# Performance work log

Hardware: AMD Instinct MI355X
Metric: run time of the kernel (lower is better)

## Reference

```python
import jax, jax.numpy as jnp
import numpy as np

N_NODES = 100000
N_EDGES = 1600000
D = 128
NUM_LAYERS = 3
BN_EPS = 1e-5


def setup_inputs() -> dict:
    key = jax.random.key(0)
    k1, k2, k3 = jax.random.split(key, 3)
    x = jax.random.normal(k1, (N_NODES, D), dtype=jnp.float32)
    edge_index = jax.random.randint(k2, (2, N_EDGES), 0, N_NODES, dtype=jnp.int32)
    # xavier-uniform-ish scale for relu gain
    scale = jnp.sqrt(2.0) * jnp.sqrt(6.0 / (D + D))
    Ws = jax.random.uniform(k3, (NUM_LAYERS, D, D), dtype=jnp.float32, minval=-1.0, maxval=1.0) * scale
    gammas = jnp.ones((NUM_LAYERS - 1, D), dtype=jnp.float32)
    betas = jnp.zeros((NUM_LAYERS - 1, D), dtype=jnp.float32)
    return {"x": x, "edge_index": edge_index, "Ws": Ws, "gammas": gammas, "betas": betas}


def gcn_conv(x, W, src, dst, num_nodes):
    # GCNConv(normalize=False, bias=False): linear then scatter-add aggregation
    h = x @ W                               # [N, D]
    msgs = h[src]                           # [E, D] irregular gather
    return jax.ops.segment_sum(msgs, dst, num_segments=num_nodes)  # [N, D] scatter-add


def batch_norm(x, gamma, beta):
    # training-mode BN over node dim, biased variance (torch semantics), deterministic
    mu = jnp.mean(x, axis=0)
    var = jnp.var(x, axis=0)
    return (x - mu) * jax.lax.rsqrt(var + BN_EPS) * gamma + beta


def reference(x, edge_index, Ws, gammas, betas):
    src, dst = edge_index[0], edge_index[1]
    n = x.shape[0]
    for i in range(NUM_LAYERS):
        x = gcn_conv(x, Ws[i], src, dst, n)
        if i != NUM_LAYERS - 1:
            x = batch_norm(x, gammas[i], betas[i])
            x = jax.nn.relu(x)
            # dropout omitted for a deterministic reference (eval-equivalent)
    return jax.nn.log_softmax(x, axis=-1)
```

## Files before the change

### kernel.cpp

```cpp
#include <hip/hip_runtime.h>

#define BN_EPS 1e-5f

typedef __attribute__((ext_vector_type(8))) short bf16x8;
typedef __attribute__((ext_vector_type(4))) float f32x4;

union VU {
    uint4 u;
    bf16x8 b;
};


__global__ __launch_bounds__(256) void hist_k(const int* __restrict__ dst, int E,
                                              int* __restrict__ ghist, int NB) {
    __shared__ int lh[128];
    if (threadIdx.x < 128) lh[threadIdx.x] = 0;
    __syncthreads();
    for (int i = blockIdx.x * 256 + threadIdx.x; i < E; i += gridDim.x * 256)
        atomicAdd(&lh[dst[i] >> 10], 1);
    __syncthreads();
    if (threadIdx.x < NB && lh[threadIdx.x]) atomicAdd(&ghist[threadIdx.x * 16], lh[threadIdx.x]);
}

__global__ __launch_bounds__(128) void pscan_k(const int* __restrict__ ghist, int NB,
                                               int* __restrict__ sbase, int* __restrict__ csrB,
                                               int* __restrict__ rowptr, int n, int E) {
    __shared__ int pa[128], pc[128];
    int t = threadIdx.x;
    int v = (t < NB) ? ghist[t * 16] : 0;
    int vp = (v + 15) & ~15;
    pa[t] = vp;
    pc[t] = v;
    __syncthreads();
    for (int s = 1; s < 128; s <<= 1) {
        int ta = (t >= s) ? pa[t - s] : 0;
        int tc = (t >= s) ? pc[t - s] : 0;
        __syncthreads();
        pa[t] += ta;
        pc[t] += tc;
        __syncthreads();
    }
    if (t < NB) {
        sbase[t] = pa[t] - vp;
        csrB[t] = pc[t] - v;
        if (t == NB - 1) {
            csrB[NB] = pc[t];
            rowptr[n] = E;
        }
    }
}

#define CHUNK 2048
__global__ __launch_bounds__(256) void bin_k(const int* __restrict__ src, const int* __restrict__ dst, int E,
                                             const int* __restrict__ sbase, int* __restrict__ snext,
                                             int* __restrict__ staged, int NB) {
    __shared__ int hist[128];
    __shared__ int base[128];
    int t = threadIdx.x;
    int c0 = blockIdx.x * CHUNK;
    if (c0 >= E) return;
    if (t < 128) hist[t] = 0;
    __syncthreads();
    int bk[8], pk[8], rk[8];
#pragma unroll
    for (int k = 0; k < 8; ++k) {
        int i = c0 + k * 256 + t;
        bk[k] = -1;
        if (i < E) {
            int d = dst[i];
            int b = d >> 10;
            bk[k] = b;
            pk[k] = src[i] | ((d & 1023) << 17);
            rk[k] = atomicAdd(&hist[b], 1);
        }
    }
    __syncthreads();
    if (t < NB) base[t] = sbase[t] + atomicAdd(&snext[t * 16], hist[t]);
    __syncthreads();
#pragma unroll
    for (int k = 0; k < 8; ++k)
        if (bk[k] >= 0) staged[base[bk[k]] + rk[k]] = pk[k];
}

__global__ __launch_bounds__(1024) void csr_k(const int* __restrict__ staged, const int* __restrict__ ghist,
                                              const int* __restrict__ sbase, const int* __restrict__ csrB,
                                              int* __restrict__ rowptr, int* __restrict__ ssrc, int n) {
    __shared__ int hist[1024], cur[1024];
    int b = blockIdx.x, t = threadIdx.x;
    int nodeBase = b << 10;
    hist[t] = 0;
    __syncthreads();
    int s0 = sbase[b], c = ghist[b * 16];
    for (int j = t; j < c; j += 1024) atomicAdd(&hist[staged[s0 + j] >> 17], 1);
    __syncthreads();
    int v = hist[t];
    for (int s = 1; s < 1024; s <<= 1) {
        int tv = (t >= s) ? hist[t - s] : 0;
        __syncthreads();
        hist[t] += tv;
        __syncthreads();
    }
    int ex = hist[t] - v;
    int cb = csrB[b];
    if (nodeBase + t < n) rowptr[nodeBase + t] = cb + ex;
    cur[t] = ex;
    __syncthreads();
    for (int j = t; j < c; j += 1024) {
        int e = staged[s0 + j];
        int p = atomicAdd(&cur[e >> 17], 1);
        ssrc[cb + p] = e & 131071;
    }
}


static __device__ __forceinline__ unsigned short f2bf(float f) {
    unsigned u = __float_as_uint(f);
    unsigned r = (u + 0x7FFFu + ((u >> 16) & 1u)) >> 16;
    return (unsigned short)r;
}
static __device__ __forceinline__ float bf_lo(unsigned u) { return __uint_as_float(u << 16); }
static __device__ __forceinline__ float bf_hi(unsigned u) { return __uint_as_float(u & 0xFFFF0000u); }


__global__ __launch_bounds__(256) void prepw_k(const float* __restrict__ Ws, uint4* __restrict__ Wp) {
    int id = blockIdx.x * 256 + threadIdx.x;
    if (id >= 3 * 4 * 8 * 64) return;
    int lane = id & 63;
    int nt = (id >> 6) & 7;
    int kt = (id >> 9) & 3;
    int L = id >> 11;
    int quad = lane >> 4, l16 = lane & 15;
    const float* wsrc = Ws + L * 16384 + (kt * 32 + quad * 8) * 128 + nt * 16 + l16;
    unsigned short s[8];
#pragma unroll
    for (int j = 0; j < 8; ++j) s[j] = f2bf(wsrc[j * 128]);
    uint4 pk;
    pk.x = (unsigned)s[0] | ((unsigned)s[1] << 16);
    pk.y = (unsigned)s[2] | ((unsigned)s[3] << 16);
    pk.z = (unsigned)s[4] | ((unsigned)s[5] << 16);
    pk.w = (unsigned)s[6] | ((unsigned)s[7] << 16);
    Wp[id] = pk;
}


template <int MODE>
__global__ __launch_bounds__(256) void mgemm_k(const float* __restrict__ Xf, const unsigned short* __restrict__ Xb,
                                               const uint4* __restrict__ Wp, unsigned short* __restrict__ H,
                                               const float* __restrict__ ss, int n) {
    int lane = threadIdx.x & 63;
    int quad = lane >> 4, l16 = lane & 15;
    int wid = (blockIdx.x * 256 + threadIdx.x) >> 6;
    int nw = (gridDim.x * 256) >> 6;
    int ntiles = (n + 15) >> 4;

    VU b[4][8];
#pragma unroll
    for (int kt = 0; kt < 4; ++kt)
#pragma unroll
        for (int nt = 0; nt < 8; ++nt) b[kt][nt].u = Wp[(kt * 8 + nt) * 64 + lane];

    auto loadA = [&](int tile, VU* a) {
        int row = tile * 16 + l16;
#pragma unroll
        for (int kt = 0; kt < 4; ++kt) {
            float f[8];
            if (MODE == 0) {
                const float* xr = Xf + (size_t)row * 128 + kt * 32 + quad * 8;
                float4 u0 = *(const float4*)(xr);
                float4 u1 = *(const float4*)(xr + 4);
                f[0] = u0.x; f[1] = u0.y; f[2] = u0.z; f[3] = u0.w;
                f[4] = u1.x; f[5] = u1.y; f[6] = u1.z; f[7] = u1.w;
            } else {
                int sl = kt * 2 + (quad >> 1);
                uint4 u = *(const uint4*)(Xb + ((size_t)sl * n + row) * 16 + (quad & 1) * 8);
                f[0] = bf_lo(u.x); f[1] = bf_hi(u.x); f[2] = bf_lo(u.y); f[3] = bf_hi(u.y);
                f[4] = bf_lo(u.z); f[5] = bf_hi(u.z); f[6] = bf_lo(u.w); f[7] = bf_hi(u.w);
                const float4* scp = (const float4*)(ss + kt * 32 + quad * 8);
                const float4* shp = (const float4*)(ss + 128 + kt * 32 + quad * 8);
                float4 c0 = scp[0], c1 = scp[1], d0 = shp[0], d1 = shp[1];
                f[0] = fmaxf(fmaf(f[0], c0.x, d0.x), 0.f);
                f[1] = fmaxf(fmaf(f[1], c0.y, d0.y), 0.f);
                f[2] = fmaxf(fmaf(f[2], c0.z, d0.z), 0.f);
                f[3] = fmaxf(fmaf(f[3], c0.w, d0.w), 0.f);
                f[4] = fmaxf(fmaf(f[4], c1.x, d1.x), 0.f);
                f[5] = fmaxf(fmaf(f[5], c1.y, d1.y), 0.f);
                f[6] = fmaxf(fmaf(f[6], c1.z, d1.z), 0.f);
                f[7] = fmaxf(fmaf(f[7], c1.w, d1.w), 0.f);
            }
            uint4 pk;
            pk.x = (unsigned)f2bf(f[0]) | ((unsigned)f2bf(f[1]) << 16);
            pk.y = (unsigned)f2bf(f[2]) | ((unsigned)f2bf(f[3]) << 16);
            pk.z = (unsigned)f2bf(f[4]) | ((unsigned)f2bf(f[5]) << 16);
            pk.w = (unsigned)f2bf(f[6]) | ((unsigned)f2bf(f[7]) << 16);
            a[kt].u = pk;
        }
    };

    int t = wid;
    VU a[4];
    if (t < ntiles) loadA(t, a);

    while (t < ntiles) {
        int tn = t + nw;
        VU an[4];
        if (tn < ntiles) loadA(tn, an);

        f32x4 acc[8];
#pragma unroll
        for (int nt = 0; nt < 8; ++nt) acc[nt] = (f32x4){0.f, 0.f, 0.f, 0.f};
#pragma unroll
        for (int kt = 0; kt < 4; ++kt)
#pragma unroll
            for (int nt = 0; nt < 8; ++nt)
                acc[nt] = __builtin_amdgcn_mfma_f32_16x16x32_bf16(b[kt][nt].b, a[kt].b, acc[nt], 0, 0, 0);

        int row = t * 16 + l16;
#pragma unroll
        for (int nt = 0; nt < 8; ++nt) {
            uint2 pk;
            pk.x = (unsigned)f2bf(acc[nt][0]) | ((unsigned)f2bf(acc[nt][1]) << 16);
            pk.y = (unsigned)f2bf(acc[nt][2]) | ((unsigned)f2bf(acc[nt][3]) << 16);
            *(uint2*)(H + ((size_t)nt * n + row) * 16 + quad * 4) = pk;
        }

#pragma unroll
        for (int kt = 0; kt < 4; ++kt) a[kt] = an[kt];
        t = tn;
    }
}


template <int MODE>
__global__ __launch_bounds__(256) void aggs_k(const unsigned short* __restrict__ H, const int* __restrict__ rowptr,
                                              const int* __restrict__ ssrc, unsigned* __restrict__ outb,
                                              float* __restrict__ outf, float* __restrict__ stats, int n) {
    __shared__ float sred[4][4][8];
    int slice = blockIdx.x & 7;
    int bg = blockIdx.x >> 3;
    int lane = threadIdx.x & 63;
    int wv = threadIdx.x >> 6;
    int g = lane >> 3;
    int f = lane & 7;
    int wid = bg * 4 + wv;
    int nwave = (gridDim.x >> 3) * 4;
    const unsigned short* hs = H + (size_t)slice * n * 16 + f * 2;
    float s0 = 0, s1 = 0, q0 = 0, q1 = 0;

    for (int base = wid * 8; base < n; base += nwave * 8) {
        int node = base + g;
        bool valid = node < n;
        int cn = valid ? node : (n - 1);
        int beg = rowptr[cn];
        int end = valid ? rowptr[cn + 1] : beg;
        float ax = 0.f, ay = 0.f;

        for (int s = 0;; s += 8) {
            if (__ballot((beg + s) < end) == 0) break;
            int idx[8];
            float sc[8];
#pragma unroll
            for (int k = 0; k < 8; ++k) {
                int j = beg + s + k;
                int cj = j < end ? j : end - 1;
                cj = cj < 0 ? 0 : cj;
                idx[k] = ssrc[cj];
                sc[k] = (j < end) ? 1.f : 0.f;
            }
            unsigned v[8];
#pragma unroll
            for (int k = 0; k < 8; ++k) v[k] = *(const unsigned*)(hs + (size_t)idx[k] * 16);
#pragma unroll
            for (int k = 0; k < 8; ++k) {
                ax = fmaf(sc[k], bf_lo(v[k]), ax);
                ay = fmaf(sc[k], bf_hi(v[k]), ay);
            }
        }

        if (MODE == 0) {
            if (valid) outb[((size_t)slice * n + node) * 8 + f] = (unsigned)f2bf(ax) | ((unsigned)f2bf(ay) << 16);
            s0 += ax; q0 += ax * ax;
            s1 += ay; q1 += ay * ay;
        } else {
            if (valid) *(float2*)(outf + (size_t)node * 128 + slice * 16 + f * 2) = make_float2(ax, ay);
        }
    }

    if (MODE == 0) {
        s0 += __shfl_xor(s0, 8); s0 += __shfl_xor(s0, 16); s0 += __shfl_xor(s0, 32);
        s1 += __shfl_xor(s1, 8); s1 += __shfl_xor(s1, 16); s1 += __shfl_xor(s1, 32);
        q0 += __shfl_xor(q0, 8); q0 += __shfl_xor(q0, 16); q0 += __shfl_xor(q0, 32);
        q1 += __shfl_xor(q1, 8); q1 += __shfl_xor(q1, 16); q1 += __shfl_xor(q1, 32);
        if (g == 0) {
            sred[wv][0][f] = s0;
            sred[wv][1][f] = s1;
            sred[wv][2][f] = q0;
            sred[wv][3][f] = q1;
        }
        __syncthreads();
        if (wv == 0 && g == 0) {
            float t0 = (sred[0][0][f] + sred[1][0][f]) + (sred[2][0][f] + sred[3][0][f]);
            float t1 = (sred[0][1][f] + sred[1][1][f]) + (sred[2][1][f] + sred[3][1][f]);
            float t2 = (sred[0][2][f] + sred[1][2][f]) + (sred[2][2][f] + sred[3][2][f]);
            float t3 = (sred[0][3][f] + sred[1][3][f]) + (sred[2][3][f] + sred[3][3][f]);
            atomicAdd(&stats[slice * 16 + 2 * f], t0);
            atomicAdd(&stats[slice * 16 + 2 * f + 1], t1);
            atomicAdd(&stats[128 + slice * 16 + 2 * f], t2);
            atomicAdd(&stats[128 + slice * 16 + 2 * f + 1], t3);
        }
    }
}


__global__ __launch_bounds__(256) void lsm_k(float* __restrict__ out, int n) {
    int lane = threadIdx.x & 63;
    int wid = (blockIdx.x * 256 + threadIdx.x) >> 6;
    int nw = (gridDim.x * 256) >> 6;
    for (int node = wid; node < n; node += nw) {
        float2 v = *(float2*)(out + (size_t)node * 128 + 2 * lane);
        float m = fmaxf(v.x, v.y);
#pragma unroll
        for (int off = 32; off > 0; off >>= 1) m = fmaxf(m, __shfl_xor(m, off));
        float ex = expf(v.x - m) + expf(v.y - m);
#pragma unroll
        for (int off = 32; off > 0; off >>= 1) ex += __shfl_xor(ex, off);
        float lse = m + logf(ex);
        *(float2*)(out + (size_t)node * 128 + 2 * lane) = make_float2(v.x - lse, v.y - lse);
    }
}


__global__ void bnfin_k(const float* __restrict__ stats, const float* __restrict__ gamma,
                        const float* __restrict__ beta, float* __restrict__ ss, int n) {
    int f = threadIdx.x;
    if (f < 128) {
        float mu = stats[f] / n;
        float var = stats[128 + f] / n - mu * mu;
        float rs = rsqrtf(fmaxf(var, 0.f) + BN_EPS);
        float sc = gamma[f] * rs;
        ss[f] = sc;
        ss[128 + f] = beta[f] - mu * sc;
    }
}


extern "C" void kernel_launch(void* const* d_in, const int* in_sizes, int n_in,
                              void* d_out, int out_size, void* d_ws, size_t ws_size,
                              hipStream_t stream) {
    const float* x = (const float*)d_in[0];
    const int* ei = (const int*)d_in[1];
    const float* Ws = (const float*)d_in[2];
    const float* gammas = (const float*)d_in[3];
    const float* betas = (const float*)d_in[4];
    int N = in_sizes[0] / 128;
    int E = in_sizes[1] / 2;
    const int* src = ei;
    const int* dst = ei + E;
    float* out = (float*)d_out;

    char* w = (char*)d_ws;
    size_t o = 0;
    auto alloc = [&](size_t bytes) { char* p = w + o; o += (bytes + 511) & ~511ull; return p; };
    unsigned short* h = (unsigned short*)alloc((size_t)N * 128 * 2);
    unsigned short* h2 = (unsigned short*)alloc((size_t)N * 128 * 2);
    int* rowptr = (int*)alloc(((size_t)N + 1) * 4);
    int* ssrc = (int*)alloc((size_t)E * 4);
    uint4* Wp = (uint4*)alloc(3 * 2048 * 16);
    float* stats = (float*)alloc(512 * 4);
    float* ss = (float*)alloc(512 * 4);

    int NB = (N + 1023) >> 10;
    int* ghist = (int*)alloc((size_t)NB * 16 * 4);
    int* snext = (int*)alloc((size_t)NB * 16 * 4);
    int* sbase = (int*)alloc((size_t)NB * 4);
    int* csrB = (int*)alloc(((size_t)NB + 1) * 4);
    int* staged = (int*)h2;

    hipMemsetAsync(ghist, 0, (size_t)NB * 16 * 4, stream);
    hipMemsetAsync(snext, 0, (size_t)NB * 16 * 4, stream);
    hipMemsetAsync(stats, 0, 512 * 4, stream);

    prepw_k<<<24, 256, 0, stream>>>(Ws, Wp);
    hist_k<<<256, 256, 0, stream>>>(dst, E, ghist, NB);
    pscan_k<<<1, 128, 0, stream>>>(ghist, NB, sbase, csrB, rowptr, N, E);
    bin_k<<<(E + CHUNK - 1) / CHUNK, 256, 0, stream>>>(src, dst, E, sbase, snext, staged, NB);
    csr_k<<<NB, 1024, 0, stream>>>(staged, ghist, sbase, csrB, rowptr, ssrc, N);

    const int AGG_BLOCKS = 2048;
    const int GEMM_BLOCKS = 512;

    mgemm_k<0><<<GEMM_BLOCKS, 256, 0, stream>>>(x, nullptr, Wp, h, nullptr, N);
    aggs_k<0><<<AGG_BLOCKS, 256, 0, stream>>>(h, rowptr, ssrc, (unsigned*)h2, nullptr, stats, N);
    bnfin_k<<<1, 128, 0, stream>>>(stats, gammas, betas, ss, N);
    mgemm_k<1><<<GEMM_BLOCKS, 256, 0, stream>>>(nullptr, h2, Wp + 2048, h, ss, N);
    aggs_k<0><<<AGG_BLOCKS, 256, 0, stream>>>(h, rowptr, ssrc, (unsigned*)h2, nullptr, stats + 256, N);
    bnfin_k<<<1, 128, 0, stream>>>(stats + 256, gammas + 128, betas + 128, ss + 256, N);
    mgemm_k<1><<<GEMM_BLOCKS, 256, 0, stream>>>(nullptr, h2, Wp + 4096, h, ss + 256, N);
    aggs_k<1><<<AGG_BLOCKS, 256, 0, stream>>>(h, rowptr, ssrc, nullptr, out, nullptr, N);
    lsm_k<<<1024, 256, 0, stream>>>(out, N);
}
```

Measured before the change: 513.3 us.

## Widen aggregation gathers to 8 bytes and cooperatively load indices via shuffles

The aggregation kernel now assigns 4 lanes per node, each gathering 4 bf16 features (8 bytes) instead of 8 lanes with 4-byte loads, so each wave handles 16 nodes at once. Neighbor indices are loaded cooperatively (one per lane), broadcast with shuffles, and prefetched one iteration ahead. The ssrc buffer gains a zero-filled pad so the over-reads stay in bounds. Together these aim to cut redundant index loads and the number of memory transactions in the gather-bound phase, at the cost of extra shuffles and possibly lower memory-level parallelism per node.

Result: slower. 564.2 us (+9.9%).

```diff
diff --git a/kernel.cpp b/kernel.cpp
--- a/kernel.cpp
+++ b/kernel.cpp
@@ -239,73 +239,88 @@
     int bg = blockIdx.x >> 3;
     int lane = threadIdx.x & 63;
     int wv = threadIdx.x >> 6;
-    int g = lane >> 3;
-    int f = lane & 7;
+    int g = lane >> 2;
+    int f4 = lane & 3;
     int wid = bg * 4 + wv;
     int nwave = (gridDim.x >> 3) * 4;
-    const unsigned short* hs = H + (size_t)slice * n * 16 + f * 2;
-    float s0 = 0, s1 = 0, q0 = 0, q1 = 0;
-
-    for (int base = wid * 8; base < n; base += nwave * 8) {
+    const unsigned* hsu = (const unsigned*)(H + (size_t)slice * n * 16) + f4 * 2;
+    int srcl = lane & ~3;
+    float s_[4] = {0.f, 0.f, 0.f, 0.f}, q_[4] = {0.f, 0.f, 0.f, 0.f};
+
+    for (int base = wid * 16; base < n; base += nwave * 16) {
         int node = base + g;
         bool valid = node < n;
         int cn = valid ? node : (n - 1);
         int beg = rowptr[cn];
         int end = valid ? rowptr[cn + 1] : beg;
-        float ax = 0.f, ay = 0.f;
-
-        for (int s = 0;; s += 8) {
-            if (__ballot((beg + s) < end) == 0) break;
-            int idx[8];
+        float a0 = 0.f, a1 = 0.f, a2 = 0.f, a3 = 0.f;
+
+        int ia = ssrc[beg + f4];
+        int ib = ssrc[beg + 4 + f4];
+        for (int s = 0;;) {
+            uint2 v[8];
             float sc[8];
 #pragma unroll
             for (int k = 0; k < 8; ++k) {
-                int j = beg + s + k;
-                int cj = j < end ? j : end - 1;
-                cj = cj < 0 ? 0 : cj;
-                idx[k] = ssrc[cj];
-                sc[k] = (j < end) ? 1.f : 0.f;
-            }
-            unsigned v[8];
-#pragma unroll
-            for (int k = 0; k < 8; ++k) v[k] = *(const unsigned*)(hs + (size_t)idx[k] * 16);
+                int idx = __shfl(k < 4 ? ia : ib, srcl + (k & 3));
+                sc[k] = (beg + s + k < end) ? 1.f : 0.f;
+                v[k] = *(const uint2*)(hsu + (((unsigned)idx) << 3));
+            }
+            int ia2 = ssrc[beg + s + 8 + f4];
+            int ib2 = ssrc[beg + s + 12 + f4];
 #pragma unroll
             for (int k = 0; k < 8; ++k) {
-                ax = fmaf(sc[k], bf_lo(v[k]), ax);
-                ay = fmaf(sc[k], bf_hi(v[k]), ay);
-            }
+                a0 = fmaf(sc[k], bf_lo(v[k].x), a0);
+                a1 = fmaf(sc[k], bf_hi(v[k].x), a1);
+                a2 = fmaf(sc[k], bf_lo(v[k].y), a2);
+                a3 = fmaf(sc[k], bf_hi(v[k].y), a3);
+            }
+            if (__ballot(beg + s + 8 < end) == 0) break;
+            ia = ia2;
+            ib = ib2;
+            s += 8;
         }
 
         if (MODE == 0) {
-            if (valid) outb[((size_t)slice * n + node) * 8 + f] = (unsigned)f2bf(ax) | ((unsigned)f2bf(ay) << 16);
-            s0 += ax; q0 += ax * ax;
-            s1 += ay; q1 += ay * ay;
+            if (valid) {
+                uint2 pk;
+                pk.x = (unsigned)f2bf(a0) | ((unsigned)f2bf(a1) << 16);
+                pk.y = (unsigned)f2bf(a2) | ((unsigned)f2bf(a3) << 16);
+                *(uint2*)(outb + ((size_t)slice * n + node) * 8 + f4 * 2) = pk;
+            }
+            s_[0] += a0; q_[0] += a0 * a0;
+            s_[1] += a1; q_[1] += a1 * a1;
+            s_[2] += a2; q_[2] += a2 * a2;
+            s_[3] += a3; q_[3] += a3 * a3;
         } else {
-            if (valid) *(float2*)(outf + (size_t)node * 128 + slice * 16 + f * 2) = make_float2(ax, ay);
+            if (valid) *(float4*)(outf + (size_t)node * 128 + slice * 16 + f4 * 4) = make_float4(a0, a1, a2, a3);
         }
     }
 
     if (MODE == 0) {
-        s0 += __shfl_xor(s0, 8); s0 += __shfl_xor(s0, 16); s0 += __shfl_xor(s0, 32);
-        s1 += __shfl_xor(s1, 8); s1 += __shfl_xor(s1, 16); s1 += __shfl_xor(s1, 32);
-        q0 += __shfl_xor(q0, 8); q0 += __shfl_xor(q0, 16); q0 += __shfl_xor(q0, 32);
-        q1 += __shfl_xor(q1, 8); q1 += __shfl_xor(q1, 16); q1 += __shfl_xor(q1, 32);
+#pragma unroll
+        for (int i = 0; i < 4; ++i) {
+            s_[i] += __shfl_xor(s_[i], 4); s_[i] += __shfl_xor(s_[i], 8);
+            s_[i] += __shfl_xor(s_[i], 16); s_[i] += __shfl_xor(s_[i], 32);
+            q_[i] += __shfl_xor(q_[i], 4); q_[i] += __shfl_xor(q_[i], 8);
+            q_[i] += __shfl_xor(q_[i], 16); q_[i] += __shfl_xor(q_[i], 32);
+        }
         if (g == 0) {
-            sred[wv][0][f] = s0;
-            sred[wv][1][f] = s1;
-            sred[wv][2][f] = q0;
-            sred[wv][3][f] = q1;
+#pragma unroll
+            for (int i = 0; i < 4; ++i) {
+                sred[wv][f4][i] = s_[i];
+                sred[wv][f4][i + 4] = q_[i];
+            }
         }
         __syncthreads();
         if (wv == 0 && g == 0) {
-            float t0 = (sred[0][0][f] + sred[1][0][f]) + (sred[2][0][f] + sred[3][0][f]);
-            float t1 = (sred[0][1][f] + sred[1][1][f]) + (sred[2][1][f] + sred[3][1][f]);
-            float t2 = (sred[0][2][f] + sred[1][2][f]) + (sred[2][2][f] + sred[3][2][f]);
-            float t3 = (sred[0][3][f] + sred[1][3][f]) + (sred[2][3][f] + sred[3][3][f]);
-            atomicAdd(&stats[slice * 16 + 2 * f], t0);
-            atomicAdd(&stats[slice * 16 + 2 * f + 1], t1);
-            atomicAdd(&stats[128 + slice * 16 + 2 * f], t2);
-            atomicAdd(&stats[128 + slice * 16 + 2 * f + 1], t3);
+#pragma unroll
+            for (int i = 0; i < 4; ++i) {
+                float ts = (sred[0][f4][i] + sred[1][f4][i]) + (sred[2][f4][i] + sred[3][f4][i]);
+                float tq = (sred[0][f4][i + 4] + sred[1][f4][i + 4]) + (sred[2][f4][i + 4] + sred[3][f4][i + 4]);
+                atomicAdd(&stats[slice * 16 + f4 * 4 + i], ts);
+                atomicAdd(&stats[128 + slice * 16 + f4 * 4 + i], tq);
+            }
         }
     }
 }
@@ -363,7 +378,7 @@
     unsigned short* h = (unsigned short*)alloc((size_t)N * 128 * 2);
     unsigned short* h2 = (unsigned short*)alloc((size_t)N * 128 * 2);
     int* rowptr = (int*)alloc(((size_t)N + 1) * 4);
-    int* ssrc = (int*)alloc((size_t)E * 4);
+    int* ssrc = (int*)alloc(((size_t)E + 128) * 4);
     uint4* Wp = (uint4*)alloc(3 * 2048 * 16);
     float* stats = (float*)alloc(512 * 4);
     float* ss = (float*)alloc(512 * 4);
@@ -378,6 +393,7 @@
     hipMemsetAsync(ghist, 0, (size_t)NB * 16 * 4, stream);
     hipMemsetAsync(snext, 0, (size_t)NB * 16 * 4, stream);
     hipMemsetAsync(stats, 0, 512 * 4, stream);
+    hipMemsetAsync(ssrc + E, 0, 128 * 4, stream);
 
     prepw_k<<<24, 256, 0, stream>>>(Ws, Wp);
     hist_k<<<256, 256, 0, stream>>>(dst, E, ghist, NB);
```

## Sort nodes by degree for balanced aggregation and prefetch next edge indices

Applied to the files above, without the earlier changes.

Adds a counting sort of nodes by in-degree (capped at 63) so each wave's 8 nodes have similar degrees, cutting divergence in the per-wave gather loop. The aggregation loop now computes the wave's max degree once and software-pipelines the ssrc index loads for the next batch while the current feature gathers are in flight. The cost is three extra small kernels, an indirection through an order array, and output writes and reads of rowptr that are no longer contiguous in node order. Padding ssrc and zeroing the tail keeps the index prefetch past the end in bounds.

Measured after the change: 621.7 us. 1.21x slower.

```diff
diff --git a/kernel.cpp b/kernel.cpp
--- a/kernel.cpp
+++ b/kernel.cpp
@@ -19,14 +19,20 @@
     for (int i = blockIdx.x * 256 + threadIdx.x; i < E; i += gridDim.x * 256)
         atomicAdd(&lh[dst[i] >> 10], 1);
     __syncthreads();
-    if (threadIdx.x < NB && lh[threadIdx.x]) atomicAdd(&ghist[threadIdx.x * 16], lh[threadIdx.x]);
+    if (threadIdx.x < 128 && threadIdx.x < NB && lh[threadIdx.x])
+        atomicAdd(&ghist[threadIdx.x * 16], lh[threadIdx.x]);
 }
 
 __global__ __launch_bounds__(128) void pscan_k(const int* __restrict__ ghist, int NB,
                                                int* __restrict__ sbase, int* __restrict__ csrB,
-                                               int* __restrict__ rowptr, int n, int E) {
+                                               int* __restrict__ rowptr, int n, int E,
+                                               int* __restrict__ dhist, int* __restrict__ dnext) {
     __shared__ int pa[128], pc[128];
     int t = threadIdx.x;
+    if (t < 64) {
+        dhist[t * 16] = 0;
+        dnext[t * 16] = 0;
+    }
     int v = (t < NB) ? ghist[t * 16] : 0;
     int vp = (v + 15) & ~15;
     pa[t] = vp;
@@ -110,6 +116,52 @@
         int p = atomicAdd(&cur[e >> 17], 1);
         ssrc[cb + p] = e & 131071;
     }
+}
+
+
+__global__ __launch_bounds__(256) void dcount_k(const int* __restrict__ rowptr, int n,
+                                                int* __restrict__ dhist) {
+    __shared__ int lh[64];
+    if (threadIdx.x < 64) lh[threadIdx.x] = 0;
+    __syncthreads();
+    for (int i = blockIdx.x * 256 + threadIdx.x; i < n; i += gridDim.x * 256) {
+        int d = rowptr[i + 1] - rowptr[i];
+        atomicAdd(&lh[min(d, 63)], 1);
+    }
+    __syncthreads();
+    if (threadIdx.x < 64 && lh[threadIdx.x]) atomicAdd(&dhist[threadIdx.x * 16], lh[threadIdx.x]);
+}
+
+__global__ void dscan_k(const int* __restrict__ dhist, int* __restrict__ dbase) {
+    int t = threadIdx.x;
+    int v = dhist[t * 16];
+    int x = v;
+#pragma unroll
+    for (int off = 1; off < 64; off <<= 1) {
+        int y = __shfl_up(x, off);
+        if (t >= off) x += y;
+    }
+    dbase[t] = x - v;
+}
+
+__global__ __launch_bounds__(1024) void dbin_k(const int* __restrict__ rowptr, int n,
+                                               const int* __restrict__ dbase, int* __restrict__ dnext,
+                                               int* __restrict__ order) {
+    __shared__ int lh[64], lbase[64];
+    int t = threadIdx.x;
+    if (t < 64) lh[t] = 0;
+    __syncthreads();
+    int i = blockIdx.x * 1024 + t;
+    int bin = -1, rk = 0;
+    if (i < n) {
+        int d = rowptr[i + 1] - rowptr[i];
+        bin = min(d, 63);
+        rk = atomicAdd(&lh[bin], 1);
+    }
+    __syncthreads();
+    if (t < 64) lbase[t] = atomicAdd(&dnext[t * 16], lh[t]);
+    __syncthreads();
+    if (i < n) order[dbase[bin] + lbase[bin] + rk] = i;
 }
 
 
@@ -232,8 +284,9 @@
 
 template <int MODE>
 __global__ __launch_bounds__(256) void aggs_k(const unsigned short* __restrict__ H, const int* __restrict__ rowptr,
-                                              const int* __restrict__ ssrc, unsigned* __restrict__ outb,
-                                              float* __restrict__ outf, float* __restrict__ stats, int n) {
+                                              const int* __restrict__ ssrc, const int* __restrict__ order,
+                                              unsigned* __restrict__ outb, float* __restrict__ outf,
+                                              float* __restrict__ stats, int n, int E) {
     __shared__ float sred[4][4][8];
     int slice = blockIdx.x & 7;
     int bg = blockIdx.x >> 3;
@@ -247,33 +300,42 @@
     float s0 = 0, s1 = 0, q0 = 0, q1 = 0;
 
     for (int base = wid * 8; base < n; base += nwave * 8) {
-        int node = base + g;
-        bool valid = node < n;
-        int cn = valid ? node : (n - 1);
-        int beg = rowptr[cn];
-        int end = valid ? rowptr[cn + 1] : beg;
+        bool valid = (base + g) < n;
+        int node = valid ? order[base + g] : 0;
+        int beg = rowptr[node];
+        int end = valid ? rowptr[node + 1] : beg;
         float ax = 0.f, ay = 0.f;
 
-        for (int s = 0;; s += 8) {
-            if (__ballot((beg + s) < end) == 0) break;
-            int idx[8];
-            float sc[8];
+        int md = end - beg;
+        md = max(md, __shfl_xor(md, 8));
+        md = max(md, __shfl_xor(md, 16));
+        md = max(md, __shfl_xor(md, 32));
+        int nb = (md + 7) >> 3;
+
+        int idx[8];
+#pragma unroll
+        for (int k = 0; k < 8; ++k) idx[k] = ssrc[beg + k];
+
+        int j0 = beg;
+        for (int it = 0; it < nb; ++it) {
+            unsigned v[8];
+#pragma unroll
+            for (int k = 0; k < 8; ++k) v[k] = *(const unsigned*)(hs + (size_t)idx[k] * 16);
+            int idn[8];
 #pragma unroll
             for (int k = 0; k < 8; ++k) {
-                int j = beg + s + k;
-                int cj = j < end ? j : end - 1;
-                cj = cj < 0 ? 0 : cj;
-                idx[k] = ssrc[cj];
-                sc[k] = (j < end) ? 1.f : 0.f;
+                int jn = j0 + 8 + k;
+                idn[k] = ssrc[jn < E ? jn : 0];
             }
-            unsigned v[8];
-#pragma unroll
-            for (int k = 0; k < 8; ++k) v[k] = *(const unsigned*)(hs + (size_t)idx[k] * 16);
 #pragma unroll
             for (int k = 0; k < 8; ++k) {
-                ax = fmaf(sc[k], bf_lo(v[k]), ax);
-                ay = fmaf(sc[k], bf_hi(v[k]), ay);
+                float sc = (j0 + k < end) ? 1.f : 0.f;
+                ax = fmaf(sc, bf_lo(v[k]), ax);
+                ay = fmaf(sc, bf_hi(v[k]), ay);
             }
+#pragma unroll
+            for (int k = 0; k < 8; ++k) idx[k] = idn[k];
+            j0 += 8;
         }
 
         if (MODE == 0) {
@@ -363,7 +425,8 @@
     unsigned short* h = (unsigned short*)alloc((size_t)N * 128 * 2);
     unsigned short* h2 = (unsigned short*)alloc((size_t)N * 128 * 2);
     int* rowptr = (int*)alloc(((size_t)N + 1) * 4);
-    int* ssrc = (int*)alloc((size_t)E * 4);
+    int* ssrc = (int*)alloc(((size_t)E + 256) * 4);
+    int* order = (int*)alloc((size_t)N * 4);
     uint4* Wp = (uint4*)alloc(3 * 2048 * 16);
     float* stats = (float*)alloc(512 * 4);
     float* ss = (float*)alloc(512 * 4);
@@ -373,28 +436,35 @@
     int* snext = (int*)alloc((size_t)NB * 16 * 4);
     int* sbase = (int*)alloc((size_t)NB * 4);
     int* csrB = (int*)alloc(((size_t)NB + 1) * 4);
+    int* dhist = (int*)alloc(64 * 16 * 4);
+    int* dnext = (int*)alloc(64 * 16 * 4);
+    int* dbase = (int*)alloc(64 * 4);
     int* staged = (int*)h2;
 
     hipMemsetAsync(ghist, 0, (size_t)NB * 16 * 4, stream);
     hipMemsetAsync(snext, 0, (size_t)NB * 16 * 4, stream);
     hipMemsetAsync(stats, 0, 512 * 4, stream);
+    hipMemsetAsync(ssrc + E, 0, 256 * 4, stream);
 
     prepw_k<<<24, 256, 0, stream>>>(Ws, Wp);
     hist_k<<<256, 256, 0, stream>>>(dst, E, ghist, NB);
-    pscan_k<<<1, 128, 0, stream>>>(ghist, NB, sbase, csrB, rowptr, N, E);
+    pscan_k<<<1, 128, 0, stream>>>(ghist, NB, sbase, csrB, rowptr, N, E, dhist, dnext);
     bin_k<<<(E + CHUNK - 1) / CHUNK, 256, 0, stream>>>(src, dst, E, sbase, snext, staged, NB);
     csr_k<<<NB, 1024, 0, stream>>>(staged, ghist, sbase, csrB, rowptr, ssrc, N);
+    dcount_k<<<128, 256, 0, stream>>>(rowptr, N, dhist);
+    dscan_k<<<1, 64, 0, stream>>>(dhist, dbase);
+    dbin_k<<<NB, 1024, 0, stream>>>(rowptr, N, dbase, dnext, order);
 
     const int AGG_BLOCKS = 2048;
     const int GEMM_BLOCKS = 512;
 
     mgemm_k<0><<<GEMM_BLOCKS, 256, 0, stream>>>(x, nullptr, Wp, h, nullptr, N);
-    aggs_k<0><<<AGG_BLOCKS, 256, 0, stream>>>(h, rowptr, ssrc, (unsigned*)h2, nullptr, stats, N);
+    aggs_k<0><<<AGG_BLOCKS, 256, 0, stream>>>(h, rowptr, ssrc, order, (unsigned*)h2, nullptr, stats, N, E);
     bnfin_k<<<1, 128, 0, stream>>>(stats, gammas, betas, ss, N);
     mgemm_k<1><<<GEMM_BLOCKS, 256, 0, stream>>>(nullptr, h2, Wp + 2048, h, ss, N);
-    aggs_k<0><<<AGG_BLOCKS, 256, 0, stream>>>(h, rowptr, ssrc, (unsigned*)h2, nullptr, stats + 256, N);
+    aggs_k<0><<<AGG_BLOCKS, 256, 0, stream>>>(h, rowptr, ssrc, order, (unsigned*)h2, nullptr, stats + 256, N, E);
     bnfin_k<<<1, 128, 0, stream>>>(stats + 256, gammas + 128, betas + 128, ss + 256, N);
     mgemm_k<1><<<GEMM_BLOCKS, 256, 0, stream>>>(nullptr, h2, Wp + 4096, h, ss + 256, N);
-    aggs_k<1><<<AGG_BLOCKS, 256, 0, stream>>>(h, rowptr, ssrc, nullptr, out, nullptr, N);
+    aggs_k<1><<<AGG_BLOCKS, 256, 0, stream>>>(h, rowptr, ssrc, order, nullptr, out, nullptr, N, E);
     lsm_k<<<1024, 256, 0, stream>>>(out, N);
 }
```
